# Optimization experiments

Hardware: AMD Instinct MI355X
Metric: run time of the kernel (lower is better)

## Reference

```python
import jax, jax.numpy as jnp
import numpy as np

V = 100000   # vocab_size
H = 128      # hidden_dim
B = 4096     # number of sentences in the batch
T = 409600


def setup_inputs() -> dict:
    key = jax.random.key(0)
    k_tok, k_seg, k_y, k_e, k_wh, k_bh, k_wo, k_bo = jax.random.split(key, 8)
    token_ids = jax.random.randint(k_tok, (T,), 0, V, dtype=jnp.int32)
    segment_ids = jnp.sort(jax.random.randint(k_seg, (T,), 0, B, dtype=jnp.int32))
    y_true = jax.random.uniform(k_y, (B,), dtype=jnp.float32)
    # learned parameters (nn.Embedding ~ N(0,1); Linear ~ U(-1/sqrt(fan_in), +))
    embed_table = jax.random.normal(k_e, (V, H), dtype=jnp.float32)
    lim = 1.0 / np.sqrt(H)
    W_hid = jax.random.uniform(k_wh, (H, H), minval=-lim, maxval=lim, dtype=jnp.float32)
    b_hid = jax.random.uniform(k_bh, (H,), minval=-lim, maxval=lim, dtype=jnp.float32)
    W_out = jax.random.uniform(k_wo, (H, 1), minval=-lim, maxval=lim, dtype=jnp.float32)
    b_out = jax.random.uniform(k_bo, (1,), minval=-lim, maxval=lim, dtype=jnp.float32)
    return {
        "token_ids": token_ids,
        "segment_ids": segment_ids,
        "y_true": y_true,
        "embed_table": embed_table,
        "W_hid": W_hid,
        "b_hid": b_hid,
        "W_out": W_out,
        "b_out": b_out,
    }


def reference(token_ids, segment_ids, y_true, embed_table, W_hid, b_hid, W_out, b_out):
    # Fused gather + segment-mean (replaces the per-sentence Python loop).
    tok_emb = embed_table[token_ids]                                    # [T, H]
    sums = jax.ops.segment_sum(tok_emb, segment_ids, num_segments=B)   # [B, H]
    counts = jax.ops.segment_sum(jnp.ones((T,), tok_emb.dtype), segment_ids,
                                 num_segments=B)                        # [B]
    sent_embeds = sums / jnp.maximum(counts, 1.0)[:, None]             # [B, H]
    # Small MLP head: tanh hidden -> sigmoid scalar score.
    hid = jnp.tanh(sent_embeds @ W_hid + b_hid)                        # [B, H]
    probas = jax.nn.sigmoid(hid @ W_out + b_out).squeeze(-1)           # [B]
    # BCE with size_average=False (sum reduction); torch clamps log at -100.
    log_p = jnp.clip(jnp.log(probas), -100.0)
    log_1mp = jnp.clip(jnp.log1p(-probas), -100.0)
    total_loss = -jnp.sum(y_true * log_p + (1.0 - y_true) * log_1mp)
    return total_loss
```

## Files before the change

### kernel.cpp

```cpp
#include <hip/hip_runtime.h>
#include <math.h>

#define HDIM 128

__global__ void seg_bounds_kernel(const int* __restrict__ seg,
                                  int* __restrict__ starts, int Tval, int Bval,
                                  float* __restrict__ out) {
    int t = blockIdx.x * blockDim.x + threadIdx.x;
    if (t >= Tval) return;
    int b = seg[t];
    int a = (t == 0) ? -1 : seg[t - 1];
    for (int s = a + 1; s <= b; ++s) starts[s] = t;
    if (t == Tval - 1)
        for (int s = b + 1; s <= Bval; ++s) starts[s] = Tval;
    if (t == 0) out[0] = 0.0f;
}

__global__ __launch_bounds__(256) void fused_dan_kernel(
    const int* __restrict__ tok, const float* __restrict__ emb,
    const int* __restrict__ starts, const float* __restrict__ Wh,
    const float* __restrict__ bh, const float* __restrict__ Wo,
    const float* __restrict__ bo, const float* __restrict__ y,
    float* __restrict__ out, int Bval) {
    __shared__ float slds[4][HDIM];
    __shared__ float lred[4];

    int wave = threadIdx.x >> 6;
    int lane = threadIdx.x & 63;
    int s = blockIdx.x * 4 + wave;
    float lsum = 0.0f;

    if (s < Bval) {
        int t0 = starts[s];
        int t1 = starts[s + 1];
        int cnt = t1 - t0;
        int half = lane >> 5;
        int col  = lane & 31;

        float4 acc = make_float4(0.f, 0.f, 0.f, 0.f);
        int i = t0 + half;

        int tix[8];
        if (i + 14 < t1) {
            #pragma unroll
            for (int k = 0; k < 8; ++k) tix[k] = tok[i + 2 * k];
        }

        while (i + 14 < t1) {
            float4 f[8];
            #pragma unroll
            for (int k = 0; k < 8; ++k)
                f[k] = ((const float4*)(emb + (size_t)tix[k] * HDIM))[col];

            int ni = i + 16;
            int ntix[8];
            if (ni + 14 < t1) {
                #pragma unroll
                for (int k = 0; k < 8; ++k) ntix[k] = tok[ni + 2 * k];
            }
            __builtin_amdgcn_sched_barrier(0);
            #pragma unroll
            for (int k = 0; k < 8; ++k) {
                acc.x += f[k].x; acc.y += f[k].y;
                acc.z += f[k].z; acc.w += f[k].w;
            }
            #pragma unroll
            for (int k = 0; k < 8; ++k) tix[k] = ntix[k];
            i = ni;
        }

        if (i < t1) {
            int lim = t1 - 1;
            int tix2[8]; float msk[8];
            #pragma unroll
            for (int k = 0; k < 8; ++k) {
                int ii = i + 2 * k;
                tix2[k] = tok[ii < lim ? ii : lim];
                msk[k] = (ii < t1) ? 1.0f : 0.0f;
            }
            float4 f[8];
            #pragma unroll
            for (int k = 0; k < 8; ++k)
                f[k] = ((const float4*)(emb + (size_t)tix2[k] * HDIM))[col];
            #pragma unroll
            for (int k = 0; k < 8; ++k) {
                acc.x = fmaf(f[k].x, msk[k], acc.x);
                acc.y = fmaf(f[k].y, msk[k], acc.y);
                acc.z = fmaf(f[k].z, msk[k], acc.z);
                acc.w = fmaf(f[k].w, msk[k], acc.w);
            }
        }

        acc.x += __shfl_down(acc.x, 32);
        acc.y += __shfl_down(acc.y, 32);
        acc.z += __shfl_down(acc.z, 32);
        acc.w += __shfl_down(acc.w, 32);

        if (half == 0) {
            float inv = 1.0f / (float)(cnt > 0 ? cnt : 1);
            acc.x *= inv; acc.y *= inv; acc.z *= inv; acc.w *= inv;
            ((float4*)&slds[wave][0])[col] = acc;
        }

        float2 bh2 = ((const float2*)bh)[lane];
        float2 wo2 = ((const float2*)Wo)[lane];
        float a0e = bh2.x, a1e = bh2.y, a0o = 0.0f, a1o = 0.0f;
        const float2* W2 = (const float2*)Wh;
        const float4* s4 = (const float4*)&slds[wave][0];
        #pragma unroll 4
        for (int q = 0; q < HDIM / 4; ++q) {
            float4 sv = s4[q];
            float2 w0 = W2[(4 * q + 0) * (HDIM / 2) + lane];
            float2 w1 = W2[(4 * q + 1) * (HDIM / 2) + lane];
            float2 w2 = W2[(4 * q + 2) * (HDIM / 2) + lane];
            float2 w3 = W2[(4 * q + 3) * (HDIM / 2) + lane];
            a0e = fmaf(sv.x, w0.x, a0e); a1e = fmaf(sv.x, w0.y, a1e);
            a0o = fmaf(sv.y, w1.x, a0o); a1o = fmaf(sv.y, w1.y, a1o);
            a0e = fmaf(sv.z, w2.x, a0e); a1e = fmaf(sv.z, w2.y, a1e);
            a0o = fmaf(sv.w, w3.x, a0o); a1o = fmaf(sv.w, w3.y, a1o);
        }
        float a0 = a0e + a0o, a1 = a1e + a1o;

        float pr = tanhf(a0) * wo2.x + tanhf(a1) * wo2.y;
        #pragma unroll
        for (int mm = 1; mm < 64; mm <<= 1) pr += __shfl_xor(pr, mm);

        if (lane == 0) {
            float z = pr + bo[0];
            float p = 1.0f / (1.0f + expf(-z));
            float lp  = fmaxf(logf(p),    -100.0f);
            float l1p = fmaxf(log1pf(-p), -100.0f);
            float yv = y[s];
            lsum = -(yv * lp + (1.0f - yv) * l1p);
        }
    }

    if (lane == 0) lred[wave] = lsum;
    __syncthreads();
    if (threadIdx.x == 0)
        atomicAdd(out, lred[0] + lred[1] + lred[2] + lred[3]);
}

extern "C" void kernel_launch(void* const* d_in, const int* in_sizes, int n_in,
                              void* d_out, int out_size, void* d_ws, size_t ws_size,
                              hipStream_t stream) {
    const int*   tok = (const int*)d_in[0];
    const int*   seg = (const int*)d_in[1];
    const float* y   = (const float*)d_in[2];
    const float* emb = (const float*)d_in[3];
    const float* Wh  = (const float*)d_in[4];
    const float* bh  = (const float*)d_in[5];
    const float* Wo  = (const float*)d_in[6];
    const float* bo  = (const float*)d_in[7];

    int T_ = in_sizes[0];
    int B_ = in_sizes[2];

    float* out = (float*)d_out;
    int* starts = (int*)d_ws;

    seg_bounds_kernel<<<(T_ + 255) / 256, 256, 0, stream>>>(seg, starts, T_, B_, out);
    fused_dan_kernel<<<(B_ + 3) / 4, 256, 0, stream>>>(tok, emb, starts, Wh, bh, Wo,
                                                       bo, y, out, B_);
}
```

Measured before the change: 131.6 us.

## Split each segment across two waves and share the hidden matvec between them

Each block now handles two sentences instead of four, and two waves gather each sentence, each taking half its tokens. Partial sums are combined through shared memory. The 128x128 hidden matvec is split by input rows between the two waves, and one wave finishes with tanh, the output projection and the BCE term. The aim is more parallelism in the memory-bound gather and a shorter serial matvec per wave. The cost is twice as many blocks, extra __syncthreads, and a launch_bounds occupancy hint.

Result: slower. 137.6 us (+4.5%).

```diff
diff --git a/kernel.cpp b/kernel.cpp
--- a/kernel.cpp
+++ b/kernel.cpp
@@ -16,45 +16,53 @@
     if (t == 0) out[0] = 0.0f;
 }
 
-__global__ __launch_bounds__(256) void fused_dan_kernel(
+__global__ __launch_bounds__(256, 8) void fused_dan_kernel(
     const int* __restrict__ tok, const float* __restrict__ emb,
     const int* __restrict__ starts, const float* __restrict__ Wh,
     const float* __restrict__ bh, const float* __restrict__ Wo,
     const float* __restrict__ bo, const float* __restrict__ y,
     float* __restrict__ out, int Bval) {
-    __shared__ float slds[4][HDIM];
-    __shared__ float lred[4];
+    __shared__ float strip[4][HDIM];
+    __shared__ float meanb[2][HDIM];
+    __shared__ float2 pm[2][64];
+    __shared__ float lred[2];
 
     int wave = threadIdx.x >> 6;
     int lane = threadIdx.x & 63;
-    int s = blockIdx.x * 4 + wave;
-    float lsum = 0.0f;
+    int segb = wave >> 1;
+    int sub  = wave & 1;
+    int s = blockIdx.x * 2 + segb;
+    bool valid = (s < Bval);
 
-    if (s < Bval) {
+    float inv = 0.0f;
+    int hw = lane >> 5, col = lane & 31;
+
+    if (valid) {
         int t0 = starts[s];
         int t1 = starts[s + 1];
         int cnt = t1 - t0;
-        int half = lane >> 5;
-        int col  = lane & 31;
+        inv = 1.0f / (float)(cnt > 0 ? cnt : 1);
+
+        int halfTok = (cnt + 1) >> 1;
+        int g0 = t0 + sub * halfTok;
+        int g1 = sub ? t1 : (t0 + halfTok);
 
         float4 acc = make_float4(0.f, 0.f, 0.f, 0.f);
-        int i = t0 + half;
+        int i = g0 + hw;
 
         int tix[8];
-        if (i + 14 < t1) {
+        if (i + 14 < g1) {
             #pragma unroll
             for (int k = 0; k < 8; ++k) tix[k] = tok[i + 2 * k];
         }
-
-        while (i + 14 < t1) {
+        while (i + 14 < g1) {
             float4 f[8];
             #pragma unroll
             for (int k = 0; k < 8; ++k)
                 f[k] = ((const float4*)(emb + (size_t)tix[k] * HDIM))[col];
-
             int ni = i + 16;
             int ntix[8];
-            if (ni + 14 < t1) {
+            if (ni + 14 < g1) {
                 #pragma unroll
                 for (int k = 0; k < 8; ++k) ntix[k] = tok[ni + 2 * k];
             }
@@ -68,15 +76,14 @@
             for (int k = 0; k < 8; ++k) tix[k] = ntix[k];
             i = ni;
         }
-
-        if (i < t1) {
-            int lim = t1 - 1;
+        if (i < g1) {
+            int lim = g1 - 1;
             int tix2[8]; float msk[8];
             #pragma unroll
             for (int k = 0; k < 8; ++k) {
                 int ii = i + 2 * k;
                 tix2[k] = tok[ii < lim ? ii : lim];
-                msk[k] = (ii < t1) ? 1.0f : 0.0f;
+                msk[k] = (ii < g1) ? 1.0f : 0.0f;
             }
             float4 f[8];
             #pragma unroll
@@ -95,36 +102,41 @@
         acc.y += __shfl_down(acc.y, 32);
         acc.z += __shfl_down(acc.z, 32);
         acc.w += __shfl_down(acc.w, 32);
+        if (hw == 0)
+            ((float4*)&strip[wave][0])[col] = acc;
+    }
+    __syncthreads();
 
-        if (half == 0) {
-            float inv = 1.0f / (float)(cnt > 0 ? cnt : 1);
-            acc.x *= inv; acc.y *= inv; acc.z *= inv; acc.w *= inv;
-            ((float4*)&slds[wave][0])[col] = acc;
+    float pa0 = 0.0f, pa1 = 0.0f;
+    if (valid) {
+        int w0 = segb * 2;
+        int idx = sub * 64 + lane;
+        float mv = (strip[w0][idx] + strip[w0 + 1][idx]) * inv;
+        meanb[segb][idx] = mv;
+
+        const float2* W2 = (const float2*)Wh;
+        int ib = sub * 64;
+        #pragma unroll 8
+        for (int q = 0; q < 64; ++q) {
+            float sv = meanb[segb][ib + q];
+            float2 w = W2[(size_t)(ib + q) * (HDIM / 2) + lane];
+            pa0 = fmaf(sv, w.x, pa0);
+            pa1 = fmaf(sv, w.y, pa1);
         }
+        if (sub == 1) pm[segb][lane] = make_float2(pa0, pa1);
+    }
+    __syncthreads();
 
+    float lsum = 0.0f;
+    if (valid && sub == 0) {
+        float2 pp = pm[segb][lane];
         float2 bh2 = ((const float2*)bh)[lane];
         float2 wo2 = ((const float2*)Wo)[lane];
-        float a0e = bh2.x, a1e = bh2.y, a0o = 0.0f, a1o = 0.0f;
-        const float2* W2 = (const float2*)Wh;
-        const float4* s4 = (const float4*)&slds[wave][0];
-        #pragma unroll 4
-        for (int q = 0; q < HDIM / 4; ++q) {
-            float4 sv = s4[q];
-            float2 w0 = W2[(4 * q + 0) * (HDIM / 2) + lane];
-            float2 w1 = W2[(4 * q + 1) * (HDIM / 2) + lane];
-            float2 w2 = W2[(4 * q + 2) * (HDIM / 2) + lane];
-            float2 w3 = W2[(4 * q + 3) * (HDIM / 2) + lane];
-            a0e = fmaf(sv.x, w0.x, a0e); a1e = fmaf(sv.x, w0.y, a1e);
-            a0o = fmaf(sv.y, w1.x, a0o); a1o = fmaf(sv.y, w1.y, a1o);
-            a0e = fmaf(sv.z, w2.x, a0e); a1e = fmaf(sv.z, w2.y, a1e);
-            a0o = fmaf(sv.w, w3.x, a0o); a1o = fmaf(sv.w, w3.y, a1o);
-        }
-        float a0 = a0e + a0o, a1 = a1e + a1o;
-
-        float pr = tanhf(a0) * wo2.x + tanhf(a1) * wo2.y;
+        float h0 = tanhf(pa0 + pp.x + bh2.x);
+        float h1 = tanhf(pa1 + pp.y + bh2.y);
+        float pr = h0 * wo2.x + h1 * wo2.y;
         #pragma unroll
         for (int mm = 1; mm < 64; mm <<= 1) pr += __shfl_xor(pr, mm);
-
         if (lane == 0) {
             float z = pr + bo[0];
             float p = 1.0f / (1.0f + expf(-z));
@@ -135,10 +147,10 @@
         }
     }
 
-    if (lane == 0) lred[wave] = lsum;
+    if (sub == 0 && lane == 0) lred[segb] = lsum;
     __syncthreads();
     if (threadIdx.x == 0)
-        atomicAdd(out, lred[0] + lred[1] + lred[2] + lred[3]);
+        atomicAdd(out, lred[0] + lred[1]);
 }
 
 extern "C" void kernel_launch(void* const* d_in, const int* in_sizes, int n_in,
@@ -160,6 +172,6 @@
     int* starts = (int*)d_ws;
 
     seg_bounds_kernel<<<(T_ + 255) / 256, 256, 0, stream>>>(seg, starts, T_, B_, out);
-    fused_dan_kernel<<<(B_ + 3) / 4, 256, 0, stream>>>(tok, emb, starts, Wh, bh, Wo,
+    fused_dan_kernel<<<(B_ + 1) / 2, 256, 0, stream>>>(tok, emb, starts, Wh, bh, Wo,
                                                        bo, y, out, B_);
 }
```

## Split hidden matvec across waves so each W_hid row is shared by four sentences

Applied to the files above, without the earlier changes.

Each wave previously read the whole 128x128 W_hid matrix for its own sentence. Now each wave reads a quarter of W_hid's rows and applies them to all four sentences in the block, writing partial sums to shared memory. Each wave then sums the four partials for its own sentence. This cuts W_hid global/L2 traffic per block fourfold, at the cost of two block-wide barriers and extra shared memory. A launch-bounds occupancy hint of 4 blocks per SM is also added.

After: 129.7 us. No clear change (-1.4%).

```diff
diff --git a/kernel.cpp b/kernel.cpp
--- a/kernel.cpp
+++ b/kernel.cpp
@@ -16,21 +16,22 @@
     if (t == 0) out[0] = 0.0f;
 }
 
-__global__ __launch_bounds__(256) void fused_dan_kernel(
+__global__ __launch_bounds__(256, 4) void fused_dan_kernel(
     const int* __restrict__ tok, const float* __restrict__ emb,
     const int* __restrict__ starts, const float* __restrict__ Wh,
     const float* __restrict__ bh, const float* __restrict__ Wo,
     const float* __restrict__ bo, const float* __restrict__ y,
     float* __restrict__ out, int Bval) {
     __shared__ float slds[4][HDIM];
+    __shared__ float2 pm[4][4][64];
     __shared__ float lred[4];
 
     int wave = threadIdx.x >> 6;
     int lane = threadIdx.x & 63;
     int s = blockIdx.x * 4 + wave;
-    float lsum = 0.0f;
+    bool valid = (s < Bval);
 
-    if (s < Bval) {
+    if (valid) {
         int t0 = starts[s];
         int t1 = starts[s + 1];
         int cnt = t1 - t0;
@@ -45,13 +46,11 @@
             #pragma unroll
             for (int k = 0; k < 8; ++k) tix[k] = tok[i + 2 * k];
         }
-
         while (i + 14 < t1) {
             float4 f[8];
             #pragma unroll
             for (int k = 0; k < 8; ++k)
                 f[k] = ((const float4*)(emb + (size_t)tix[k] * HDIM))[col];
-
             int ni = i + 16;
             int ntix[8];
             if (ni + 14 < t1) {
@@ -68,7 +67,6 @@
             for (int k = 0; k < 8; ++k) tix[k] = ntix[k];
             i = ni;
         }
-
         if (i < t1) {
             int lim = t1 - 1;
             int tix2[8]; float msk[8];
@@ -101,30 +99,49 @@
             acc.x *= inv; acc.y *= inv; acc.z *= inv; acc.w *= inv;
             ((float4*)&slds[wave][0])[col] = acc;
         }
+    } else {
+        if (lane < 32)
+            ((float4*)&slds[wave][0])[lane] = make_float4(0.f, 0.f, 0.f, 0.f);
+    }
+    __syncthreads();
 
+    {
+        const float2* W2 = (const float2*)Wh;
+        float2 p0 = make_float2(0.f, 0.f), p1 = p0, p2 = p0, p3 = p0;
+        int qb = wave * 32;
+        #pragma unroll 4
+        for (int q = 0; q < 32; ++q) {
+            int row = qb + q;
+            float2 w = W2[(size_t)row * (HDIM / 2) + lane];
+            float s0 = slds[0][row];
+            float s1 = slds[1][row];
+            float s2 = slds[2][row];
+            float s3 = slds[3][row];
+            p0.x = fmaf(s0, w.x, p0.x); p0.y = fmaf(s0, w.y, p0.y);
+            p1.x = fmaf(s1, w.x, p1.x); p1.y = fmaf(s1, w.y, p1.y);
+            p2.x = fmaf(s2, w.x, p2.x); p2.y = fmaf(s2, w.y, p2.y);
+            p3.x = fmaf(s3, w.x, p3.x); p3.y = fmaf(s3, w.y, p3.y);
+        }
+        pm[wave][0][lane] = p0;
+        pm[wave][1][lane] = p1;
+        pm[wave][2][lane] = p2;
+        pm[wave][3][lane] = p3;
+    }
+    __syncthreads();
+
+    float lsum = 0.0f;
+    if (valid) {
+        float2 q0 = pm[0][wave][lane];
+        float2 q1 = pm[1][wave][lane];
+        float2 q2 = pm[2][wave][lane];
+        float2 q3 = pm[3][wave][lane];
         float2 bh2 = ((const float2*)bh)[lane];
         float2 wo2 = ((const float2*)Wo)[lane];
-        float a0e = bh2.x, a1e = bh2.y, a0o = 0.0f, a1o = 0.0f;
-        const float2* W2 = (const float2*)Wh;
-        const float4* s4 = (const float4*)&slds[wave][0];
-        #pragma unroll 4
-        for (int q = 0; q < HDIM / 4; ++q) {
-            float4 sv = s4[q];
-            float2 w0 = W2[(4 * q + 0) * (HDIM / 2) + lane];
-            float2 w1 = W2[(4 * q + 1) * (HDIM / 2) + lane];
-            float2 w2 = W2[(4 * q + 2) * (HDIM / 2) + lane];
-            float2 w3 = W2[(4 * q + 3) * (HDIM / 2) + lane];
-            a0e = fmaf(sv.x, w0.x, a0e); a1e = fmaf(sv.x, w0.y, a1e);
-            a0o = fmaf(sv.y, w1.x, a0o); a1o = fmaf(sv.y, w1.y, a1o);
-            a0e = fmaf(sv.z, w2.x, a0e); a1e = fmaf(sv.z, w2.y, a1e);
-            a0o = fmaf(sv.w, w3.x, a0o); a1o = fmaf(sv.w, w3.y, a1o);
-        }
-        float a0 = a0e + a0o, a1 = a1e + a1o;
-
+        float a0 = q0.x + q1.x + q2.x + q3.x + bh2.x;
+        float a1 = q0.y + q1.y + q2.y + q3.y + bh2.y;
         float pr = tanhf(a0) * wo2.x + tanhf(a1) * wo2.y;
         #pragma unroll
         for (int mm = 1; mm < 64; mm <<= 1) pr += __shfl_xor(pr, mm);
-
         if (lane == 0) {
             float z = pr + bo[0];
             float p = 1.0f / (1.0f + expf(-z));
```
